# Kernel optimization log

Measured on AMD Instinct MI355X. Metric: run time of the kernel, lower is better.

The kernel has to match this reference:

```python
import jax, jax.numpy as jnp
import numpy as np

EPS = 1e-5


def setup_inputs() -> dict:
    key = jax.random.key(0)
    kx, ky = jax.random.split(key)
    n, d, num_classes = 32768, 128, 64
    x = jax.random.normal(kx, (n, d), dtype=jnp.float32)
    y = jax.random.randint(ky, (n,), 0, num_classes, dtype=jnp.int64)
    return {"x": x, "y": y, "num_classes": num_classes}


def reference(x, y, num_classes):
    n, d = x.shape
    m = n // 2
    x_support, x_target = x[:m], x[m:]
    y_support, y_target = y[:m], y[m:]

    # prototypes: scatter-add instead of one-hot multiply+sum (same math)
    class_counts = jax.ops.segment_sum(
        jnp.ones((m,), x.dtype), y_support, num_segments=num_classes)
    class_counts = class_counts + (class_counts < 0.01).astype(x.dtype)
    prototypes = jax.ops.segment_sum(
        x_support, y_support, num_segments=num_classes) / class_counts[:, None]

    # broadcast distance with the module's custom 'square'
    diff = x_target[:, None, :] - prototypes[None, :, :]  # (m, C, d)
    sq = jnp.sign(diff) * jnp.exp(2.0 * jnp.log(jnp.abs(diff + EPS)))
    distance = -jnp.mean(sq, axis=2)  # (m, C) logits

    # cross entropy (mean over batch)
    logp = jax.nn.log_softmax(distance, axis=1)
    loss = -jnp.take_along_axis(logp, y_target[:, None], axis=1).mean()
    return loss
```

## Files before the change

### kernel.cpp

```cpp
#include <hip/hip_runtime.h>

#define M_HALF 16384
#define D 128
#define C 64

#define K1_BLOCKS 256
#define K1_ROWS 64

#define K2_BLOCKS 256

#define K3_BLOCKS 256
#define K3_ROWS 64

__global__ __launch_bounds__(256) void k1_partials(
    const float* __restrict__ x, const int* __restrict__ y,
    float* __restrict__ partials)
{
    const int tid  = threadIdx.x;
    const int lane = tid & 63;
    const int kq   = tid >> 6;
    const int base = blockIdx.x * K1_ROWS;

    const int ycl = y[base + lane];
    unsigned long long mymask = 0ULL;
    for (int ci = 0; ci < C; ++ci) {
        const unsigned long long m = __ballot(ycl == ci);
        if (lane == ci) mymask = m;
    }

    float acc[32];
    #pragma unroll
    for (int j = 0; j < 32; ++j) acc[j] = 0.f;
    unsigned long long m = mymask;
    while (m) {
        const int r = (int)__builtin_ctzll(m);
        m &= m - 1;
        const float4* xr = (const float4*)(x + (size_t)(base + r) * D + kq * 32);
        #pragma unroll
        for (int j4 = 0; j4 < 8; ++j4) {
            const float4 v = xr[j4];
            acc[j4*4+0] += v.x; acc[j4*4+1] += v.y;
            acc[j4*4+2] += v.z; acc[j4*4+3] += v.w;
        }
    }

    float* outp = partials + (size_t)blockIdx.x * (C * D) + (kq * 64 + lane) * 32;
    #pragma unroll
    for (int j4 = 0; j4 < 8; ++j4)
        *(float4*)&outp[j4 * 4] =
            make_float4(acc[j4*4], acc[j4*4+1], acc[j4*4+2], acc[j4*4+3]);
}

__global__ __launch_bounds__(256) void k2_finalize(
    const float* __restrict__ partials, const int* __restrict__ y,
    float* __restrict__ pTg,
    float* __restrict__ out)
{
    __shared__ float red[8][33];
    __shared__ int   cred[4];
    const int tid = threadIdx.x;
    const int blk = blockIdx.x;
    const int myc = blk & 63;

    int cnt = 0;
    const int4* y4 = (const int4*)y;
    #pragma unroll 4
    for (int i = tid; i < M_HALF / 4; i += 256) {
        const int4 v = y4[i];
        cnt += (v.x == myc) + (v.y == myc) + (v.z == myc) + (v.w == myc);
    }
    #pragma unroll
    for (int off = 32; off; off >>= 1) cnt += __shfl_xor(cnt, off);
    if ((tid & 63) == 0) cred[tid >> 6] = cnt;

    if (blk == 0 && tid == 65) out[0] = 0.f;

    const int sub  = tid >> 5;
    const int pidx = tid & 31;
    const int q    = blk * 32 + pidx;
    float s = 0.f;
    const int b0 = sub * 32;
    #pragma unroll 8
    for (int i = 0; i < 32; ++i)
        s += partials[(size_t)(b0 + i) * (C * D) + q];
    red[sub][pidx] = s;
    __syncthreads();

    if (tid < 32) {
        float tot = 0.f;
        #pragma unroll
        for (int u = 0; u < 8; ++u) tot += red[u][tid];
        float c = (float)(cred[0] + cred[1] + cred[2] + cred[3]);
        if (c < 0.5f) c = 1.f;
        tot /= c;
        const int k = (blk >> 6) * 32 + tid;
        pTg[((k >> 2) * 64 + (myc & 3) * 16 + (myc >> 2)) * 4 + (k & 3)] = tot;
    }
}

__global__ __launch_bounds__(256) void k3_dist_loss(
    const float* __restrict__ x, const int* __restrict__ y,
    const float4* __restrict__ pTg4,
    float* __restrict__ out)
{
    __shared__ float4 pT4[32 * 64];
    __shared__ float  wsum[4];
    const int tid = threadIdx.x;

    for (int o = tid; o < 32 * 64; o += 256) pT4[o] = pTg4[o];
    __syncthreads();

    const int lane = tid & 63;
    const int wid  = tid >> 6;
    const int cg   = lane & 15;
    const int rg   = lane >> 4;
    const int rbase = wid * 16 + rg * 4;
    const int row0 = M_HALF + blockIdx.x * K3_ROWS;

    const float4* xrow[4];
    #pragma unroll
    for (int r = 0; r < 4; ++r)
        xrow[r] = (const float4*)(x + (size_t)(row0 + rbase + r) * D);

    float acc[4][4];
    #pragma unroll
    for (int r = 0; r < 4; ++r)
        #pragma unroll
        for (int cc = 0; cc < 4; ++cc) acc[r][cc] = 0.f;

    #pragma unroll 2
    for (int k4 = 0; k4 < 32; ++k4) {
        float4 pv[4], xv[4];
        #pragma unroll
        for (int cc = 0; cc < 4; ++cc) pv[cc] = pT4[k4 * 64 + cc * 16 + cg];
        #pragma unroll
        for (int r = 0; r < 4; ++r) xv[r] = xrow[r][k4];
        #pragma unroll
        for (int r = 0; r < 4; ++r) {
            #pragma unroll
            for (int cc = 0; cc < 4; ++cc) {
                float d;
                d = xv[r].x - pv[cc].x; acc[r][cc] = fmaf(d, fabsf(d), acc[r][cc]);
                d = xv[r].y - pv[cc].y; acc[r][cc] = fmaf(d, fabsf(d), acc[r][cc]);
                d = xv[r].z - pv[cc].z; acc[r][cc] = fmaf(d, fabsf(d), acc[r][cc]);
                d = xv[r].w - pv[cc].w; acc[r][cc] = fmaf(d, fabsf(d), acc[r][cc]);
            }
        }
    }

    const float ninv_d = -1.f / (float)D;
    float lsum = 0.f;
    #pragma unroll
    for (int r = 0; r < 4; ++r) {
        float dv0 = acc[r][0] * ninv_d, dv1 = acc[r][1] * ninv_d;
        float dv2 = acc[r][2] * ninv_d, dv3 = acc[r][3] * ninv_d;
        float mx = fmaxf(fmaxf(dv0, dv1), fmaxf(dv2, dv3));
        #pragma unroll
        for (int off = 8; off; off >>= 1) mx = fmaxf(mx, __shfl_xor(mx, off));
        float se = __expf(dv0 - mx) + __expf(dv1 - mx) +
                   __expf(dv2 - mx) + __expf(dv3 - mx);
        #pragma unroll
        for (int off = 8; off; off >>= 1) se += __shfl_xor(se, off);
        const float lse = mx + __logf(se);

        const int yt  = y[row0 + rbase + r];
        const int cct = yt & 3, cgt = yt >> 2;
        const float v01 = (cct & 1) ? dv1 : dv0;
        const float v23 = (cct & 1) ? dv3 : dv2;
        const float val = (cct & 2) ? v23 : v01;
        const float dy  = __shfl(val, (lane & 48) | cgt);
        lsum += lse - dy;
    }

    lsum += __shfl_xor(lsum, 16);
    lsum += __shfl_xor(lsum, 32);

    if (lane == 0) wsum[wid] = lsum;
    __syncthreads();
    if (tid == 0) {
        const float tot = (wsum[0] + wsum[1] + wsum[2] + wsum[3]) * (1.f / (float)M_HALF);
        atomicAdd(out, tot);
    }
}

extern "C" void kernel_launch(void* const* d_in, const int* in_sizes, int n_in,
                              void* d_out, int out_size, void* d_ws, size_t ws_size,
                              hipStream_t stream) {
    const float* x = (const float*)d_in[0];
    const int*   y = (const int*)d_in[1];
    float* out = (float*)d_out;

    float* ws_f     = (float*)d_ws;
    float* pTg      = ws_f;
    float* partials = pTg + D * C;

    k1_partials<<<K1_BLOCKS, 256, 0, stream>>>(x, y, partials);
    k2_finalize<<<K2_BLOCKS, 256, 0, stream>>>(partials, y, pTg, out);
    k3_dist_loss<<<K3_BLOCKS, 256, 0, stream>>>(x, y, (const float4*)pTg, out);
}
```

Baseline: 37.87 us.

## Fuse three kernels into one persistent kernel with atomic grid barriers

Merges the partial-sum, finalize and distance/loss kernels into a single launch of 256 blocks. Two software grid barriers, built from an atomic counter with sleep polling, separate the stages, and a memset resets the counter before each launch. This removes two kernel launch gaps, but it assumes all 256 blocks are resident at once and adds barrier latency plus a memset call. The spin loops have a guard limit, so if a block is not resident the wait times out and later stages may read incomplete data.

```diff
diff --git a/kernel.cpp b/kernel.cpp
--- a/kernel.cpp
+++ b/kernel.cpp
@@ -3,183 +3,193 @@
 #define M_HALF 16384
 #define D 128
 #define C 64
-
-#define K1_BLOCKS 256
-#define K1_ROWS 64
-
-#define K2_BLOCKS 256
-
-#define K3_BLOCKS 256
+#define NBLK 256
+#define NTHR 256
 #define K3_ROWS 64
 
-__global__ __launch_bounds__(256) void k1_partials(
+__global__ __launch_bounds__(NTHR) void fused_proto_loss(
     const float* __restrict__ x, const int* __restrict__ y,
-    float* __restrict__ partials)
-{
-    const int tid  = threadIdx.x;
-    const int lane = tid & 63;
-    const int kq   = tid >> 6;
-    const int base = blockIdx.x * K1_ROWS;
-
-    const int ycl = y[base + lane];
-    unsigned long long mymask = 0ULL;
-    for (int ci = 0; ci < C; ++ci) {
-        const unsigned long long m = __ballot(ycl == ci);
-        if (lane == ci) mymask = m;
-    }
-
-    float acc[32];
-    #pragma unroll
-    for (int j = 0; j < 32; ++j) acc[j] = 0.f;
-    unsigned long long m = mymask;
-    while (m) {
-        const int r = (int)__builtin_ctzll(m);
-        m &= m - 1;
-        const float4* xr = (const float4*)(x + (size_t)(base + r) * D + kq * 32);
-        #pragma unroll
-        for (int j4 = 0; j4 < 8; ++j4) {
-            const float4 v = xr[j4];
-            acc[j4*4+0] += v.x; acc[j4*4+1] += v.y;
-            acc[j4*4+2] += v.z; acc[j4*4+3] += v.w;
-        }
-    }
-
-    float* outp = partials + (size_t)blockIdx.x * (C * D) + (kq * 64 + lane) * 32;
-    #pragma unroll
-    for (int j4 = 0; j4 < 8; ++j4)
-        *(float4*)&outp[j4 * 4] =
-            make_float4(acc[j4*4], acc[j4*4+1], acc[j4*4+2], acc[j4*4+3]);
-}
-
-__global__ __launch_bounds__(256) void k2_finalize(
-    const float* __restrict__ partials, const int* __restrict__ y,
+    float* __restrict__ partials,
     float* __restrict__ pTg,
-    float* __restrict__ out)
-{
-    __shared__ float red[8][33];
-    __shared__ int   cred[4];
-    const int tid = threadIdx.x;
-    const int blk = blockIdx.x;
-    const int myc = blk & 63;
-
-    int cnt = 0;
-    const int4* y4 = (const int4*)y;
-    #pragma unroll 4
-    for (int i = tid; i < M_HALF / 4; i += 256) {
-        const int4 v = y4[i];
-        cnt += (v.x == myc) + (v.y == myc) + (v.z == myc) + (v.w == myc);
-    }
-    #pragma unroll
-    for (int off = 32; off; off >>= 1) cnt += __shfl_xor(cnt, off);
-    if ((tid & 63) == 0) cred[tid >> 6] = cnt;
-
-    if (blk == 0 && tid == 65) out[0] = 0.f;
-
-    const int sub  = tid >> 5;
-    const int pidx = tid & 31;
-    const int q    = blk * 32 + pidx;
-    float s = 0.f;
-    const int b0 = sub * 32;
-    #pragma unroll 8
-    for (int i = 0; i < 32; ++i)
-        s += partials[(size_t)(b0 + i) * (C * D) + q];
-    red[sub][pidx] = s;
-    __syncthreads();
-
-    if (tid < 32) {
-        float tot = 0.f;
-        #pragma unroll
-        for (int u = 0; u < 8; ++u) tot += red[u][tid];
-        float c = (float)(cred[0] + cred[1] + cred[2] + cred[3]);
-        if (c < 0.5f) c = 1.f;
-        tot /= c;
-        const int k = (blk >> 6) * 32 + tid;
-        pTg[((k >> 2) * 64 + (myc & 3) * 16 + (myc >> 2)) * 4 + (k & 3)] = tot;
-    }
-}
-
-__global__ __launch_bounds__(256) void k3_dist_loss(
-    const float* __restrict__ x, const int* __restrict__ y,
-    const float4* __restrict__ pTg4,
+    int*   __restrict__ syncCnt,
     float* __restrict__ out)
 {
     __shared__ float4 pT4[32 * 64];
+    __shared__ float  red[8][33];
+    __shared__ int    cred[4];
     __shared__ float  wsum[4];
-    const int tid = threadIdx.x;
-
-    for (int o = tid; o < 32 * 64; o += 256) pT4[o] = pTg4[o];
-    __syncthreads();
-
+
+    const int tid  = threadIdx.x;
     const int lane = tid & 63;
-    const int wid  = tid >> 6;
-    const int cg   = lane & 15;
-    const int rg   = lane >> 4;
-    const int rbase = wid * 16 + rg * 4;
-    const int row0 = M_HALF + blockIdx.x * K3_ROWS;
-
-    const float4* xrow[4];
-    #pragma unroll
-    for (int r = 0; r < 4; ++r)
-        xrow[r] = (const float4*)(x + (size_t)(row0 + rbase + r) * D);
-
-    float acc[4][4];
-    #pragma unroll
-    for (int r = 0; r < 4; ++r)
-        #pragma unroll
-        for (int cc = 0; cc < 4; ++cc) acc[r][cc] = 0.f;
-
-    #pragma unroll 2
-    for (int k4 = 0; k4 < 32; ++k4) {
-        float4 pv[4], xv[4];
-        #pragma unroll
-        for (int cc = 0; cc < 4; ++cc) pv[cc] = pT4[k4 * 64 + cc * 16 + cg];
-        #pragma unroll
-        for (int r = 0; r < 4; ++r) xv[r] = xrow[r][k4];
+    const int blk  = blockIdx.x;
+
+    {
+        const int kq   = tid >> 6;
+        const int base = blk * 64;
+        const int ycl  = y[base + lane];
+        unsigned long long mymask = 0ULL;
+        for (int ci = 0; ci < C; ++ci) {
+            const unsigned long long m = __ballot(ycl == ci);
+            if (lane == ci) mymask = m;
+        }
+        float acc[32];
+        #pragma unroll
+        for (int j = 0; j < 32; ++j) acc[j] = 0.f;
+        unsigned long long m = mymask;
+        while (m) {
+            const int r = (int)__builtin_ctzll(m);
+            m &= m - 1;
+            const float4* xr = (const float4*)(x + (size_t)(base + r) * D + kq * 32);
+            #pragma unroll
+            for (int j4 = 0; j4 < 8; ++j4) {
+                const float4 v = xr[j4];
+                acc[j4*4+0] += v.x; acc[j4*4+1] += v.y;
+                acc[j4*4+2] += v.z; acc[j4*4+3] += v.w;
+            }
+        }
+        float* outp = partials + (size_t)blk * (C * D) + (kq * 64 + lane) * 32;
+        #pragma unroll
+        for (int j4 = 0; j4 < 8; ++j4)
+            *(float4*)&outp[j4 * 4] =
+                make_float4(acc[j4*4], acc[j4*4+1], acc[j4*4+2], acc[j4*4+3]);
+        if (blk == 0 && tid == 0) out[0] = 0.f;
+    }
+
+    __syncthreads();
+    if (tid == 0) {
+        __threadfence();
+        atomicAdd(syncCnt, 1);
+        int guard = 0;
+        while (atomicAdd(syncCnt, 0) < NBLK && guard < (1 << 26)) {
+            __builtin_amdgcn_s_sleep(2); ++guard;
+        }
+        __threadfence();
+    }
+    __syncthreads();
+
+    {
+        const int myc = blk & 63;
+        int cnt = 0;
+        const int4* y4 = (const int4*)y;
+        #pragma unroll 4
+        for (int i = tid; i < M_HALF / 4; i += NTHR) {
+            const int4 v = y4[i];
+            cnt += (v.x == myc) + (v.y == myc) + (v.z == myc) + (v.w == myc);
+        }
+        #pragma unroll
+        for (int off = 32; off; off >>= 1) cnt += __shfl_xor(cnt, off);
+        if ((tid & 63) == 0) cred[tid >> 6] = cnt;
+
+        const int sub  = tid >> 5;
+        const int pidx = tid & 31;
+        const int q    = blk * 32 + pidx;
+        float s = 0.f;
+        const int b0 = sub * 32;
+        #pragma unroll 8
+        for (int i = 0; i < 32; ++i)
+            s += partials[(size_t)(b0 + i) * (C * D) + q];
+        red[sub][pidx] = s;
+        __syncthreads();
+
+        if (tid < 32) {
+            float tot = 0.f;
+            #pragma unroll
+            for (int u = 0; u < 8; ++u) tot += red[u][tid];
+            float c = (float)(cred[0] + cred[1] + cred[2] + cred[3]);
+            if (c < 0.5f) c = 1.f;
+            tot /= c;
+            const int k = (blk >> 6) * 32 + tid;
+            pTg[((k >> 2) * 64 + (myc & 3) * 16 + (myc >> 2)) * 4 + (k & 3)] = tot;
+        }
+    }
+
+    __syncthreads();
+    if (tid == 0) {
+        __threadfence();
+        atomicAdd(syncCnt, 1);
+        int guard = 0;
+        while (atomicAdd(syncCnt, 0) < 2 * NBLK && guard < (1 << 26)) {
+            __builtin_amdgcn_s_sleep(2); ++guard;
+        }
+        __threadfence();
+    }
+    __syncthreads();
+
+    {
+        const float4* pTg4 = (const float4*)pTg;
+        for (int o = tid; o < 32 * 64; o += NTHR) pT4[o] = pTg4[o];
+        __syncthreads();
+
+        const int wid  = tid >> 6;
+        const int cg   = lane & 15;
+        const int rg   = lane >> 4;
+        const int rbase = wid * 16 + rg * 4;
+        const int row0 = M_HALF + blk * K3_ROWS;
+
+        const float4* xrow[4];
+        #pragma unroll
+        for (int r = 0; r < 4; ++r)
+            xrow[r] = (const float4*)(x + (size_t)(row0 + rbase + r) * D);
+
+        float acc[4][4];
+        #pragma unroll
+        for (int r = 0; r < 4; ++r)
+            #pragma unroll
+            for (int cc = 0; cc < 4; ++cc) acc[r][cc] = 0.f;
+
+        #pragma unroll 2
+        for (int k4 = 0; k4 < 32; ++k4) {
+            float4 pv[4], xv[4];
+            #pragma unroll
+            for (int cc = 0; cc < 4; ++cc) pv[cc] = pT4[k4 * 64 + cc * 16 + cg];
+            #pragma unroll
+            for (int r = 0; r < 4; ++r) xv[r] = xrow[r][k4];
+            #pragma unroll
+            for (int r = 0; r < 4; ++r) {
+                #pragma unroll
+                for (int cc = 0; cc < 4; ++cc) {
+                    float d;
+                    d = xv[r].x - pv[cc].x; acc[r][cc] = fmaf(d, fabsf(d), acc[r][cc]);
+                    d = xv[r].y - pv[cc].y; acc[r][cc] = fmaf(d, fabsf(d), acc[r][cc]);
+                    d = xv[r].z - pv[cc].z; acc[r][cc] = fmaf(d, fabsf(d), acc[r][cc]);
+                    d = xv[r].w - pv[cc].w; acc[r][cc] = fmaf(d, fabsf(d), acc[r][cc]);
+                }
+            }
+        }
+
+        const float ninv_d = -1.f / (float)D;
+        float lsum = 0.f;
         #pragma unroll
         for (int r = 0; r < 4; ++r) {
-            #pragma unroll
-            for (int cc = 0; cc < 4; ++cc) {
-                float d;
-                d = xv[r].x - pv[cc].x; acc[r][cc] = fmaf(d, fabsf(d), acc[r][cc]);
-                d = xv[r].y - pv[cc].y; acc[r][cc] = fmaf(d, fabsf(d), acc[r][cc]);
-                d = xv[r].z - pv[cc].z; acc[r][cc] = fmaf(d, fabsf(d), acc[r][cc]);
-                d = xv[r].w - pv[cc].w; acc[r][cc] = fmaf(d, fabsf(d), acc[r][cc]);
-            }
-        }
-    }
-
-    const float ninv_d = -1.f / (float)D;
-    float lsum = 0.f;
-    #pragma unroll
-    for (int r = 0; r < 4; ++r) {
-        float dv0 = acc[r][0] * ninv_d, dv1 = acc[r][1] * ninv_d;
-        float dv2 = acc[r][2] * ninv_d, dv3 = acc[r][3] * ninv_d;
-        float mx = fmaxf(fmaxf(dv0, dv1), fmaxf(dv2, dv3));
-        #pragma unroll
-        for (int off = 8; off; off >>= 1) mx = fmaxf(mx, __shfl_xor(mx, off));
-        float se = __expf(dv0 - mx) + __expf(dv1 - mx) +
-                   __expf(dv2 - mx) + __expf(dv3 - mx);
-        #pragma unroll
-        for (int off = 8; off; off >>= 1) se += __shfl_xor(se, off);
-        const float lse = mx + __logf(se);
-
-        const int yt  = y[row0 + rbase + r];
-        const int cct = yt & 3, cgt = yt >> 2;
-        const float v01 = (cct & 1) ? dv1 : dv0;
-        const float v23 = (cct & 1) ? dv3 : dv2;
-        const float val = (cct & 2) ? v23 : v01;
-        const float dy  = __shfl(val, (lane & 48) | cgt);
-        lsum += lse - dy;
-    }
-
-    lsum += __shfl_xor(lsum, 16);
-    lsum += __shfl_xor(lsum, 32);
-
-    if (lane == 0) wsum[wid] = lsum;
-    __syncthreads();
-    if (tid == 0) {
-        const float tot = (wsum[0] + wsum[1] + wsum[2] + wsum[3]) * (1.f / (float)M_HALF);
-        atomicAdd(out, tot);
+            float dv0 = acc[r][0] * ninv_d, dv1 = acc[r][1] * ninv_d;
+            float dv2 = acc[r][2] * ninv_d, dv3 = acc[r][3] * ninv_d;
+            float mx = fmaxf(fmaxf(dv0, dv1), fmaxf(dv2, dv3));
+            #pragma unroll
+            for (int off = 8; off; off >>= 1) mx = fmaxf(mx, __shfl_xor(mx, off));
+            float se = __expf(dv0 - mx) + __expf(dv1 - mx) +
+                       __expf(dv2 - mx) + __expf(dv3 - mx);
+            #pragma unroll
+            for (int off = 8; off; off >>= 1) se += __shfl_xor(se, off);
+            const float lse = mx + __logf(se);
+
+            const int yt  = y[row0 + rbase + r];
+            const int cct = yt & 3, cgt = yt >> 2;
+            const float v01 = (cct & 1) ? dv1 : dv0;
+            const float v23 = (cct & 1) ? dv3 : dv2;
+            const float val = (cct & 2) ? v23 : v01;
+            const float dy  = __shfl(val, (lane & 48) | cgt);
+            lsum += lse - dy;
+        }
+
+        lsum += __shfl_xor(lsum, 16);
+        lsum += __shfl_xor(lsum, 32);
+
+        if (lane == 0) wsum[wid] = lsum;
+        __syncthreads();
+        if (tid == 0) {
+            const float tot = (wsum[0] + wsum[1] + wsum[2] + wsum[3]) * (1.f / (float)M_HALF);
+            atomicAdd(out, tot);
+        }
     }
 }
 
@@ -191,10 +201,10 @@
     float* out = (float*)d_out;
 
     float* ws_f     = (float*)d_ws;
-    float* pTg      = ws_f;
+    int*   syncCnt  = (int*)ws_f;
+    float* pTg      = ws_f + 64;
     float* partials = pTg + D * C;
 
-    k1_partials<<<K1_BLOCKS, 256, 0, stream>>>(x, y, partials);
-    k2_finalize<<<K2_BLOCKS, 256, 0, stream>>>(partials, y, pTg, out);
-    k3_dist_loss<<<K3_BLOCKS, 256, 0, stream>>>(x, y, (const float4*)pTg, out);
+    hipMemsetAsync(syncCnt, 0, sizeof(int), stream);
+    fused_proto_loss<<<NBLK, NTHR, 0, stream>>>(x, y, partials, pTg, syncCnt, out);
 }
```

New measurement: 85.22 us. 2.25x slower.

## Fuse prototype partials and finalize into one per-class kernel; prefetch x in distance loop

Applied to the files above, without the earlier changes.

Replaces the two-kernel prototype computation (per-block partial sums written to a 2 MB workspace, then a reduction kernel) with a single kernel. Each block owns one class and a 16-column slice, scans all support labels, and accumulates matching rows directly. This removes one launch and the partials round-trip through memory. In exchange, every block re-reads the full label array and does scattered, divergent row loads, so y is read 512 times. The distance kernel also software-prefetches the next x float4 per row to overlap global loads with compute.

```diff
diff --git a/kernel.cpp b/kernel.cpp
--- a/kernel.cpp
+++ b/kernel.cpp
@@ -4,101 +4,69 @@
 #define D 128
 #define C 64
 
-#define K1_BLOCKS 256
-#define K1_ROWS 64
+#define KP_BLOCKS 512
+#define KC_BLOCKS 256
+#define KC_ROWS 64
 
-#define K2_BLOCKS 256
-
-#define K3_BLOCKS 256
-#define K3_ROWS 64
-
-__global__ __launch_bounds__(256) void k1_partials(
+__global__ __launch_bounds__(256) void kp_proto(
     const float* __restrict__ x, const int* __restrict__ y,
-    float* __restrict__ partials)
+    float* __restrict__ pTg,
+    float* __restrict__ out)
 {
+    __shared__ float red[4][16];
+    __shared__ int   credw[4];
     const int tid  = threadIdx.x;
     const int lane = tid & 63;
-    const int kq   = tid >> 6;
-    const int base = blockIdx.x * K1_ROWS;
+    const int wid  = tid >> 6;
+    const int blk  = blockIdx.x;
+    const int myc  = blk & 63;
+    const int kq8  = blk >> 6;
 
-    const int ycl = y[base + lane];
-    unsigned long long mymask = 0ULL;
-    for (int ci = 0; ci < C; ++ci) {
-        const unsigned long long m = __ballot(ycl == ci);
-        if (lane == ci) mymask = m;
-    }
+    if (blk == 0 && tid == 0) out[0] = 0.f;
 
-    float acc[32];
+    float acc[16];
     #pragma unroll
-    for (int j = 0; j < 32; ++j) acc[j] = 0.f;
-    unsigned long long m = mymask;
-    while (m) {
-        const int r = (int)__builtin_ctzll(m);
-        m &= m - 1;
-        const float4* xr = (const float4*)(x + (size_t)(base + r) * D + kq * 32);
-        #pragma unroll
-        for (int j4 = 0; j4 < 8; ++j4) {
-            const float4 v = xr[j4];
-            acc[j4*4+0] += v.x; acc[j4*4+1] += v.y;
-            acc[j4*4+2] += v.z; acc[j4*4+3] += v.w;
+    for (int j = 0; j < 16; ++j) acc[j] = 0.f;
+    int cnt = 0;
+
+    const float* xbase = x + kq8 * 16;
+    #pragma unroll 4
+    for (int r = tid; r < M_HALF; r += 256) {
+        if (y[r] == myc) {
+            ++cnt;
+            const float4* xr = (const float4*)(xbase + (size_t)r * D);
+            #pragma unroll
+            for (int j4 = 0; j4 < 4; ++j4) {
+                const float4 v = xr[j4];
+                acc[j4*4+0] += v.x; acc[j4*4+1] += v.y;
+                acc[j4*4+2] += v.z; acc[j4*4+3] += v.w;
+            }
         }
     }
 
-    float* outp = partials + (size_t)blockIdx.x * (C * D) + (kq * 64 + lane) * 32;
     #pragma unroll
-    for (int j4 = 0; j4 < 8; ++j4)
-        *(float4*)&outp[j4 * 4] =
-            make_float4(acc[j4*4], acc[j4*4+1], acc[j4*4+2], acc[j4*4+3]);
-}
-
-__global__ __launch_bounds__(256) void k2_finalize(
-    const float* __restrict__ partials, const int* __restrict__ y,
-    float* __restrict__ pTg,
-    float* __restrict__ out)
-{
-    __shared__ float red[8][33];
-    __shared__ int   cred[4];
-    const int tid = threadIdx.x;
-    const int blk = blockIdx.x;
-    const int myc = blk & 63;
-
-    int cnt = 0;
-    const int4* y4 = (const int4*)y;
-    #pragma unroll 4
-    for (int i = tid; i < M_HALF / 4; i += 256) {
-        const int4 v = y4[i];
-        cnt += (v.x == myc) + (v.y == myc) + (v.z == myc) + (v.w == myc);
+    for (int off = 32; off; off >>= 1) {
+        #pragma unroll
+        for (int j = 0; j < 16; ++j) acc[j] += __shfl_xor(acc[j], off);
+        cnt += __shfl_xor(cnt, off);
     }
-    #pragma unroll
-    for (int off = 32; off; off >>= 1) cnt += __shfl_xor(cnt, off);
-    if ((tid & 63) == 0) cred[tid >> 6] = cnt;
-
-    if (blk == 0 && tid == 65) out[0] = 0.f;
-
-    const int sub  = tid >> 5;
-    const int pidx = tid & 31;
-    const int q    = blk * 32 + pidx;
-    float s = 0.f;
-    const int b0 = sub * 32;
-    #pragma unroll 8
-    for (int i = 0; i < 32; ++i)
-        s += partials[(size_t)(b0 + i) * (C * D) + q];
-    red[sub][pidx] = s;
+    if (lane == 0) {
+        #pragma unroll
+        for (int j = 0; j < 16; ++j) red[wid][j] = acc[j];
+        credw[wid] = cnt;
+    }
     __syncthreads();
-
-    if (tid < 32) {
-        float tot = 0.f;
-        #pragma unroll
-        for (int u = 0; u < 8; ++u) tot += red[u][tid];
-        float c = (float)(cred[0] + cred[1] + cred[2] + cred[3]);
+    if (tid < 16) {
+        float tot = red[0][tid] + red[1][tid] + red[2][tid] + red[3][tid];
+        float c = (float)(credw[0] + credw[1] + credw[2] + credw[3]);
         if (c < 0.5f) c = 1.f;
         tot /= c;
-        const int k = (blk >> 6) * 32 + tid;
+        const int k = kq8 * 16 + tid;
         pTg[((k >> 2) * 64 + (myc & 3) * 16 + (myc >> 2)) * 4 + (k & 3)] = tot;
     }
 }
 
-__global__ __launch_bounds__(256) void k3_dist_loss(
+__global__ __launch_bounds__(256) void kc_dist_loss(
     const float* __restrict__ x, const int* __restrict__ y,
     const float4* __restrict__ pTg4,
     float* __restrict__ out)
@@ -115,7 +83,7 @@
     const int cg   = lane & 15;
     const int rg   = lane >> 4;
     const int rbase = wid * 16 + rg * 4;
-    const int row0 = M_HALF + blockIdx.x * K3_ROWS;
+    const int row0 = M_HALF + blockIdx.x * KC_ROWS;
 
     const float4* xrow[4];
     #pragma unroll
@@ -128,13 +96,19 @@
         #pragma unroll
         for (int cc = 0; cc < 4; ++cc) acc[r][cc] = 0.f;
 
-    #pragma unroll 2
+    float4 xv[4], xvn[4];
+    #pragma unroll
+    for (int r = 0; r < 4; ++r) xv[r] = xrow[r][0];
+
+    #pragma unroll 4
     for (int k4 = 0; k4 < 32; ++k4) {
-        float4 pv[4], xv[4];
+        if (k4 < 31) {
+            #pragma unroll
+            for (int r = 0; r < 4; ++r) xvn[r] = xrow[r][k4 + 1];
+        }
+        float4 pv[4];
         #pragma unroll
         for (int cc = 0; cc < 4; ++cc) pv[cc] = pT4[k4 * 64 + cc * 16 + cg];
-        #pragma unroll
-        for (int r = 0; r < 4; ++r) xv[r] = xrow[r][k4];
         #pragma unroll
         for (int r = 0; r < 4; ++r) {
             #pragma unroll
@@ -146,6 +120,8 @@
                 d = xv[r].w - pv[cc].w; acc[r][cc] = fmaf(d, fabsf(d), acc[r][cc]);
             }
         }
+        #pragma unroll
+        for (int r = 0; r < 4; ++r) xv[r] = xvn[r];
     }
 
     const float ninv_d = -1.f / (float)D;
@@ -190,11 +166,8 @@
     const int*   y = (const int*)d_in[1];
     float* out = (float*)d_out;
 
-    float* ws_f     = (float*)d_ws;
-    float* pTg      = ws_f;
-    float* partials = pTg + D * C;
+    float* pTg = (float*)d_ws;
 
-    k1_partials<<<K1_BLOCKS, 256, 0, stream>>>(x, y, partials);
-    k2_finalize<<<K2_BLOCKS, 256, 0, stream>>>(partials, y, pTg, out);
-    k3_dist_loss<<<K3_BLOCKS, 256, 0, stream>>>(x, y, (const float4*)pTg, out);
+    kp_proto<<<KP_BLOCKS, 256, 0, stream>>>(x, y, pTg, out);
+    kc_dist_loss<<<KC_BLOCKS, 256, 0, stream>>>(x, y, (const float4*)pTg, out);
 }
```

After: 40.64 us. +7.3%, slower.
